# Performance work log

Hardware: AMD Instinct MI355X
Metric: run time of the kernel (lower is better)

The kernel has to match this reference:

```python
import jax, jax.numpy as jnp
import numpy as np

N = 100000          # number of nodes
E = 128             # embedding size
NUM_LAYERS = 4
SMOOTH = 12.0       # MAXIMUM_SMOOTHNESS
RELATIONS = [("at", 2), ("clear", 1), ("on", 2)]  # sorted, as in module
ATOM_COUNTS = {"at": 150000, "clear": 150000, "on": 150000}


def mish(x):
    return x * jnp.tanh(jax.nn.softplus(x))


def _linear_init(k, din, dout):
    s = 1.0 / np.sqrt(din)
    kw, kb = jax.random.split(k)
    w = jax.random.uniform(kw, (din, dout), jnp.float32, -s, s)
    b = jax.random.uniform(kb, (dout,), jnp.float32, -s, s)
    return w, b


def setup_inputs() -> dict:
    key = jax.random.key(0)
    ks = iter(jax.random.split(key, 64))
    inp = {}
    inp["node_embeddings"] = jax.random.normal(next(ks), (N, E), jnp.float32)
    for name, ar in RELATIONS:
        inp[f"atoms_{name}"] = jax.random.randint(
            next(ks), (ATOM_COUNTS[name] * ar,), 0, N, dtype=jnp.int32)
        d = ar * E
        inp[f"w_in_{name}"], inp[f"b_in_{name}"] = _linear_init(next(ks), d, d)
        inp[f"w_out_{name}"], inp[f"b_out_{name}"] = _linear_init(next(ks), d, d)
    # update MLP: Linear(2E, 2E) -> mish -> Linear(2E, E)
    inp["w_u_in"], inp["b_u_in"] = _linear_init(next(ks), 2 * E, 2 * E)
    inp["w_u_out"], inp["b_u_out"] = _linear_init(next(ks), 2 * E, E)
    return inp


def _forward(node_embeddings, atoms, params):
    w_u_in, b_u_in, w_u_out, b_u_out = params["update"]

    def layer(h):
        msgs, idxs = [], []
        for name, ar in RELATIONS:
            w_in, b_in, w_out, b_out = params[name]
            av = atoms[name]                              # [A*ar] node indices
            x = h[av].reshape(-1, ar * E)                 # gather -> [A, ar*E]
            y = x + (mish(x @ w_in + b_in) @ w_out + b_out)  # residual MLP
            msgs.append(y.reshape(-1, E))
            idxs.append(av)
        msg = jnp.concatenate(msgs, 0)                    # [T, E]
        idx = jnp.concatenate(idxs, 0)                    # [T]
        # smooth-max aggregation (max offsets are not differentiated)
        seg_max = jax.ops.segment_max(msg, idx, num_segments=N)
        seg_max = jnp.where(jnp.isfinite(seg_max), seg_max, 0.0)  # empty -> 0 (include_self=False on zeros)
        seg_max = jax.lax.stop_gradient(seg_max)
        exps = jnp.exp(SMOOTH * (msg - seg_max[idx]))
        exps_sum = jax.ops.segment_sum(exps, idx, num_segments=N) + 1e-16
        max_msg = jnp.log(exps_sum) / SMOOTH + seg_max
        upd_in = jnp.concatenate([max_msg, h], axis=1)    # [N, 2E]
        upd = mish(upd_in @ w_u_in + b_u_in) @ w_u_out + b_u_out
        return h + upd                                    # outer residual

    h = node_embeddings
    for _ in range(NUM_LAYERS):
        h = layer(h)
    return h


def reference(node_embeddings, atoms_at, atoms_clear, atoms_on,
              w_in_at, b_in_at, w_out_at, b_out_at,
              w_in_clear, b_in_clear, w_out_clear, b_out_clear,
              w_in_on, b_in_on, w_out_on, b_out_on,
              w_u_in, b_u_in, w_u_out, b_u_out):
    atoms = {"at": atoms_at, "clear": atoms_clear, "on": atoms_on}
    params = {
        "at": (w_in_at, b_in_at, w_out_at, b_out_at),
        "clear": (w_in_clear, b_in_clear, w_out_clear, b_out_clear),
        "on": (w_in_on, b_in_on, w_out_on, b_out_on),
        "update": (w_u_in, b_u_in, w_u_out, b_u_out),
    }
    return _forward(node_embeddings, atoms, params)
```

## Files before the change

### kernel.cpp

```cpp
#include <hip/hip_runtime.h>
#include <hip/hip_bf16.h>
#include <math.h>

#define NNODES 100000
#define EDIM 128
#define TSLOTS 750000
#define NB 391
#define GRA 2344

typedef __bf16 bf16x8 __attribute__((ext_vector_type(8)));
typedef __bf16 bf16x4 __attribute__((ext_vector_type(4)));
typedef float f32x4 __attribute__((ext_vector_type(4)));
typedef unsigned int u32x4 __attribute__((ext_vector_type(4)));

#define T_SCALE 17.312340490667562f
#define INV_SCALE 0.05776226504666211f
#define EMPTY_V (-3.0701134f)

__device__ __forceinline__ float mishf(float x) {
  float u = __expf(fminf(x, 15.f));
  float num = u * (u + 2.f);
  return x * num * __builtin_amdgcn_rcpf(num + 2.f);
}

__device__ __forceinline__ double exp12t(float t) {
  t = fmaxf(t, -20000.f);
  float ti = floorf(t);
  float m = exp2f(t - ti);
  int ei = (int)ti;
  ei = ei < -1000 ? -1000 : (ei > 1000 ? 1000 : ei);
  return (double)m * __longlong_as_double(((long long)(1023 + ei)) << 52);
}

__device__ __forceinline__ float logS12(double S) {
  if (!(S > 0.0)) return EMPTY_V;
  long long b = __double_as_longlong(S);
  int e2 = (int)((b >> 52) & 0x7FF) - 1023;
  float mf = __uint_as_float(0x3F800000u | (unsigned)((b >> 29) & 0x7FFFFF));
  return ((float)e2 + log2f(mf)) * INV_SCALE;
}

__global__ void k_sentinel(float* out, int n) {
  int i = blockIdx.x * 256 + threadIdx.x;
  if (i < n) out[i] = 1.0e6f;
}

__global__ void k_init(const float* __restrict__ h0, __bf16* __restrict__ hb, int n8) {
  int i = blockIdx.x * 256 + threadIdx.x;
  if (i >= n8) return;
  float4 f0 = ((const float4*)h0)[i * 2];
  float4 f1 = ((const float4*)h0)[i * 2 + 1];
  bf16x8 p = {(__bf16)f0.x, (__bf16)f0.y, (__bf16)f0.z, (__bf16)f0.w,
              (__bf16)f1.x, (__bf16)f1.y, (__bf16)f1.z, (__bf16)f1.w};
  *(bf16x8*)(hb + (size_t)i * 8) = p;
}

struct TransDesc {
  const float* src[8];
  __bf16* dst[8];
  int R[8];
  int C[8];
  int tstart[9];
};

__global__ void k_transpose_all(TransDesc td) {
  __shared__ float tile[32][33];
  int b = blockIdx.x;
  int m = 0;
  while (m < 7 && b >= td.tstart[m + 1]) m++;
  int t = b - td.tstart[m];
  int R = td.R[m], C = td.C[m];
  int tcols = C >> 5;
  int by = t / tcols, bx = t - by * tcols;
  int tx = threadIdx.x & 31, ty = threadIdx.x >> 5;
  const float* src = td.src[m];
  __bf16* dst = td.dst[m];
  for (int i = 0; i < 32; i += 8)
    tile[ty + i][tx] = src[(size_t)(by * 32 + ty + i) * C + bx * 32 + tx];
  __syncthreads();
  for (int i = 0; i < 32; i += 8)
    dst[(size_t)(bx * 32 + ty + i) * R + by * 32 + tx] = (__bf16)tile[tx][ty + i];
}

__device__ __forceinline__ int slot_node(int s, const int* at, const int* cl, const int* on) {
  if (s < 300000) return at[s];
  if (s < 450000) return cl[s - 300000];
  return on[s - 450000];
}

__global__ void k_count(const int* __restrict__ at, const int* __restrict__ cl,
                        const int* __restrict__ on, int* __restrict__ cnt) {
  int s = blockIdx.x * 256 + threadIdx.x;
  if (s >= TSLOTS) return;
  atomicAdd(&cnt[slot_node(s, at, cl, on)], 1);
}

__global__ void k_bsum(const int* __restrict__ cnt, int* __restrict__ bsum) {
  __shared__ int sm[256];
  int n = blockIdx.x * 256 + threadIdx.x;
  sm[threadIdx.x] = (n < NNODES) ? cnt[n] : 0;
  __syncthreads();
  for (int st = 128; st > 0; st >>= 1) {
    if (threadIdx.x < st) sm[threadIdx.x] += sm[threadIdx.x + st];
    __syncthreads();
  }
  if (threadIdx.x == 0) bsum[blockIdx.x] = sm[0];
}

__global__ void k_bscan(const int* __restrict__ bsum, int* __restrict__ bpre,
                        int* __restrict__ off) {
  __shared__ int sm[512];
  int t = threadIdx.x;
  int v = (t < NB) ? bsum[t] : 0;
  sm[t] = v;
  __syncthreads();
  for (int st = 1; st < 512; st <<= 1) {
    int x = (t >= st) ? sm[t - st] : 0;
    __syncthreads();
    sm[t] += x;
    __syncthreads();
  }
  if (t < NB) bpre[t] = sm[t] - v;
  if (t == NB - 1) off[NNODES] = sm[t];
}

__global__ void k_off(const int* __restrict__ cnt, const int* __restrict__ bpre,
                      int* __restrict__ off) {
  __shared__ int sm[256];
  int n = blockIdx.x * 256 + threadIdx.x;
  int v = (n < NNODES) ? cnt[n] : 0;
  sm[threadIdx.x] = v;
  __syncthreads();
  for (int st = 1; st < 256; st <<= 1) {
    int t = (threadIdx.x >= st) ? sm[threadIdx.x - st] : 0;
    __syncthreads();
    sm[threadIdx.x] += t;
    __syncthreads();
  }
  if (n < NNODES) off[n] = bpre[blockIdx.x] + sm[threadIdx.x] - v;
}

__global__ void k_fill(const int* __restrict__ at, const int* __restrict__ cl,
                       const int* __restrict__ on, const int* __restrict__ off,
                       int* __restrict__ cnt, int* __restrict__ perm) {
  int s = blockIdx.x * 256 + threadIdx.x;
  if (s >= TSLOTS) return;
  int node = slot_node(s, at, cl, on);
  int pos = atomicAdd(&cnt[node], -1) - 1;
  perm[s] = off[node] + pos;
}

struct RelAll {
  const int* av[3];
  const __bf16* wt1[3];
  const float* b1[3];
  const __bf16* wt2[3];
  const float* b2[3];
  const int* prm[3];
};

__global__ __launch_bounds__(512, 6) void k_relf(
    const float* __restrict__ hf, const __bf16* __restrict__ hb,
    RelAll ra, _Float16* __restrict__ msg) {
  __shared__ __align__(16) __bf16 xs[64][264];
  __shared__ int prm[128];
  const int tid = threadIdx.x;
  const int lane = tid & 63;
  const int w = tid >> 6;
  const int b = blockIdx.x;
  const int m = (b < GRA) ? 0 : (b < 2 * GRA ? 1 : 2);
  const int row0 = (b - m * GRA) * 64;
  const int A = 150000;
  const int* av = ra.av[m];
  const __bf16* wt1 = ra.wt1[m];
  const float* b1 = ra.b1[m];
  const __bf16* wt2 = ra.wt2[m];
  const float* b2 = ra.b2[m];
  const int* permrel = ra.prm[m];
  const int lhi = lane >> 4, llo = lane & 15;
  ushort* zs = (ushort*)&xs[0][0];

  if (m < 2) {
    if (tid < 128) {
      int i2 = row0 * 2 + tid;
      prm[tid] = (i2 < 2 * A) ? permrel[i2] : 0;
    }
    if (hb != nullptr) {
      for (int i = 0; i < 4; ++i) {
        int s = tid + i * 512;
        int r = s >> 5, o = s & 31;
        int a = row0 + r;
        uint4 v = {0, 0, 0, 0};
        if (a < A) {
          int node = av[2 * a + (o >> 4)];
          v = *(const uint4*)(hb + (size_t)node * 128 + (o & 15) * 8);
        }
        *(uint4*)&xs[r][o * 8] = v;
      }
    } else {
      for (int i = 0; i < 8; ++i) {
        int s = tid + i * 512;
        int r = s >> 6, o = s & 63;
        int a = row0 + r;
        float4 f = {0.f, 0.f, 0.f, 0.f};
        if (a < A) {
          int node = av[2 * a + (o >> 5)];
          f = *(const float4*)(hf + (size_t)node * 128 + (o & 31) * 4);
        }
        bf16x4 p = {(__bf16)f.x, (__bf16)f.y, (__bf16)f.z, (__bf16)f.w};
        *(bf16x4*)&xs[r][o * 4] = p;
      }
    }
    __syncthreads();

    const int cb = w * 32;
    f32x4 acc1[4][2];
#pragma unroll
    for (int rt = 0; rt < 4; rt++)
#pragma unroll
      for (int ct = 0; ct < 2; ct++) acc1[rt][ct] = (f32x4){0.f, 0.f, 0.f, 0.f};
#pragma unroll
    for (int kk = 0; kk < 8; ++kk) {
      int k = kk * 32 + lhi * 8;
      bf16x8 af[4], bfr[2];
#pragma unroll
      for (int rt = 0; rt < 4; rt++) af[rt] = *(const bf16x8*)&xs[rt * 16 + llo][k];
#pragma unroll
      for (int ct = 0; ct < 2; ct++)
        bfr[ct] = *(const bf16x8*)(wt1 + (size_t)(cb + ct * 16 + llo) * 256 + k);
#pragma unroll
      for (int rt = 0; rt < 4; rt++)
#pragma unroll
        for (int ct = 0; ct < 2; ct++)
          acc1[rt][ct] = __builtin_amdgcn_mfma_f32_16x16x32_bf16(af[rt], bfr[ct], acc1[rt][ct], 0, 0, 0);
    }
    __syncthreads();

    float b1v[2];
#pragma unroll
    for (int ct = 0; ct < 2; ct++) b1v[ct] = b1[cb + ct * 16 + llo];
#pragma unroll
    for (int rt = 0; rt < 4; rt++)
#pragma unroll
      for (int ct = 0; ct < 2; ct++)
#pragma unroll
        for (int i = 0; i < 4; i++)
          xs[rt * 16 + lhi * 4 + i][cb + ct * 16 + llo] = (__bf16)mishf(acc1[rt][ct][i] + b1v[ct]);
    __syncthreads();

    f32x4 acc2[4][2];
#pragma unroll
    for (int rt = 0; rt < 4; rt++)
#pragma unroll
      for (int ct = 0; ct < 2; ct++) acc2[rt][ct] = (f32x4){0.f, 0.f, 0.f, 0.f};
#pragma unroll
    for (int kk = 0; kk < 8; ++kk) {
      int k = kk * 32 + lhi * 8;
      bf16x8 af[4], bfr[2];
#pragma unroll
      for (int rt = 0; rt < 4; rt++) af[rt] = *(const bf16x8*)&xs[rt * 16 + llo][k];
#pragma unroll
      for (int ct = 0; ct < 2; ct++)
        bfr[ct] = *(const bf16x8*)(wt2 + (size_t)(cb + ct * 16 + llo) * 256 + k);
#pragma unroll
      for (int rt = 0; rt < 4; rt++)
#pragma unroll
        for (int ct = 0; ct < 2; ct++)
          acc2[rt][ct] = __builtin_amdgcn_mfma_f32_16x16x32_bf16(af[rt], bfr[ct], acc2[rt][ct], 0, 0, 0);
    }
    __syncthreads();

    float b2v[2];
#pragma unroll
    for (int ct = 0; ct < 2; ct++) b2v[ct] = b2[cb + ct * 16 + llo];
#pragma unroll
    for (int rt = 0; rt < 4; rt++)
#pragma unroll
      for (int ct = 0; ct < 2; ct++)
#pragma unroll
        for (int i = 0; i < 4; i++) {
          int r = rt * 16 + lhi * 4 + i;
          int col = cb + ct * 16 + llo;
          union { ushort u; _Float16 f; } cv;
          cv.f = (_Float16)(acc2[rt][ct][i] + b2v[ct]);
          zs[r * 264 + col] = cv.u;
        }
    __syncthreads();

    for (int i = 0; i < 4; ++i) {
      int s = tid + i * 512;
      int sr = s >> 4;
      int c = s & 15;
      int a = row0 + (sr >> 1);
      if (a < A) {
        int rr = sr >> 1, c0 = (sr & 1) * 128 + c * 8;
        u32x4 z = *(const u32x4*)&zs[rr * 264 + c0];
        __builtin_nontemporal_store(z, (u32x4*)(msg + (size_t)prm[sr] * 128 + c * 8));
      }
    }
  } else {
    if (tid < 64) {
      int a = row0 + tid;
      prm[tid] = (a < A) ? permrel[a] : 0;
    }
    if (hb != nullptr) {
      for (int i = 0; i < 2; ++i) {
        int s = tid + i * 512;
        int r = s >> 4, o = s & 15;
        int a = row0 + r;
        uint4 v = {0, 0, 0, 0};
        if (a < A) {
          int node = av[a];
          v = *(const uint4*)(hb + (size_t)node * 128 + o * 8);
        }
        *(uint4*)&xs[r][o * 8] = v;
      }
    } else {
      for (int i = 0; i < 4; ++i) {
        int s = tid + i * 512;
        int r = s >> 5, o = s & 31;
        int a = row0 + r;
        float4 f = {0.f, 0.f, 0.f, 0.f};
        if (a < A) {
          int node = av[a];
          f = *(const float4*)(hf + (size_t)node * 128 + o * 4);
        }
        bf16x4 p = {(__bf16)f.x, (__bf16)f.y, (__bf16)f.z, (__bf16)f.w};
        *(bf16x4*)&xs[r][o * 4] = p;
      }
    }
    __syncthreads();

    const int cb = w * 16;
    f32x4 acc1[4];
#pragma unroll
    for (int rt = 0; rt < 4; rt++) acc1[rt] = (f32x4){0.f, 0.f, 0.f, 0.f};
#pragma unroll
    for (int kk = 0; kk < 4; ++kk) {
      int k = kk * 32 + lhi * 8;
      bf16x8 af[4], bfr;
#pragma unroll
      for (int rt = 0; rt < 4; rt++) af[rt] = *(const bf16x8*)&xs[rt * 16 + llo][k];
      bfr = *(const bf16x8*)(wt1 + (size_t)(cb + llo) * 128 + k);
#pragma unroll
      for (int rt = 0; rt < 4; rt++)
        acc1[rt] = __builtin_amdgcn_mfma_f32_16x16x32_bf16(af[rt], bfr, acc1[rt], 0, 0, 0);
    }
    __syncthreads();

    float b1v = b1[cb + llo];
#pragma unroll
    for (int rt = 0; rt < 4; rt++)
#pragma unroll
      for (int i = 0; i < 4; i++)
        xs[rt * 16 + lhi * 4 + i][cb + llo] = (__bf16)mishf(acc1[rt][i] + b1v);
    __syncthreads();

    f32x4 acc2[4];
#pragma unroll
    for (int rt = 0; rt < 4; rt++) acc2[rt] = (f32x4){0.f, 0.f, 0.f, 0.f};
#pragma unroll
    for (int kk = 0; kk < 4; ++kk) {
      int k = kk * 32 + lhi * 8;
      bf16x8 af[4], bfr;
#pragma unroll
      for (int rt = 0; rt < 4; rt++) af[rt] = *(const bf16x8*)&xs[rt * 16 + llo][k];
      bfr = *(const bf16x8*)(wt2 + (size_t)(cb + llo) * 128 + k);
#pragma unroll
      for (int rt = 0; rt < 4; rt++)
        acc2[rt] = __builtin_amdgcn_mfma_f32_16x16x32_bf16(af[rt], bfr, acc2[rt], 0, 0, 0);
    }
    __syncthreads();

    float b2v = b2[cb + llo];
#pragma unroll
    for (int rt = 0; rt < 4; rt++)
#pragma unroll
      for (int i = 0; i < 4; i++) {
        int r = rt * 16 + lhi * 4 + i;
        int col = cb + llo;
        union { ushort u; _Float16 f; } cv;
        cv.f = (_Float16)(acc2[rt][i] + b2v);
        zs[r * 264 + col] = cv.u;
      }
    __syncthreads();

    for (int i = 0; i < 2; ++i) {
      int s = tid + i * 512;
      int sr = s >> 4;
      int c = s & 15;
      int a = row0 + sr;
      if (a < A) {
        u32x4 z = *(const u32x4*)&zs[sr * 264 + c * 8];
        __builtin_nontemporal_store(z, (u32x4*)(msg + (size_t)prm[sr] * 128 + c * 8));
      }
    }
  }
}

__global__ __launch_bounds__(512, 6) void k_aggmlp(
    const _Float16* __restrict__ msg, const int* __restrict__ off,
    const float* __restrict__ hin, const __bf16* __restrict__ hb,
    const __bf16* __restrict__ wt1, const float* __restrict__ b1,
    const __bf16* __restrict__ wt2, const float* __restrict__ b2,
    float* __restrict__ hout, __bf16* __restrict__ hbout) {
  __shared__ __align__(16) __bf16 xs[64][264];
  __shared__ int offs[65];
  const int tid = threadIdx.x;
  const int lane = tid & 63;
  const int w = tid >> 6;
  const int node0 = blockIdx.x * 64;
  const bool useb = (hbout != nullptr);

  if (tid < 65) {
    int n = node0 + tid;
    offs[tid] = off[n < NNODES ? n : NNODES];
  }
  if (useb) {
    for (int i = 0; i < 2; ++i) {
      int s = tid + i * 512;
      int r = s >> 4, o = s & 15;
      int n = node0 + r;
      uint4 v = {0, 0, 0, 0};
      if (n < NNODES) v = *(const uint4*)(hb + (size_t)n * 128 + o * 8);
      *(uint4*)&xs[r][128 + o * 8] = v;
    }
  } else {
    for (int i = 0; i < 4; ++i) {
      int s = tid + i * 512;
      int r = s >> 5, o = s & 31;
      int n = node0 + r;
      float4 f = {0.f, 0.f, 0.f, 0.f};
      if (n < NNODES) f = *(const float4*)(hin + (size_t)n * 128 + o * 4);
      bf16x4 p = {(__bf16)f.x, (__bf16)f.y, (__bf16)f.z, (__bf16)f.w};
      *(bf16x4*)&xs[r][128 + o * 4] = p;
    }
  }
  if (node0 + 64 > NNODES) {
    for (int s = tid; s < 64 * 16; s += 512) {
      int r = s >> 4, o = s & 15;
      if (node0 + r >= NNODES) *(uint4*)&xs[r][o * 8] = (uint4){0, 0, 0, 0};
    }
  }
  __syncthreads();

  const int rg = lane >> 4;
  const int fl = lane & 15;
  const _Float16* mb = msg + fl * 8;

#pragma unroll 1
  for (int j = 0; j < 8; ++j) {
    int n = node0 + w * 8 + j;
    if (n >= NNODES) break;
    float h[8];
    if (useb) {
      bf16x8 hq = *(const bf16x8*)(hb + (size_t)n * 128 + fl * 8);
#pragma unroll
      for (int k = 0; k < 8; ++k) h[k] = (float)hq[k];
    } else {
      float4 a0 = *(const float4*)(hin + (size_t)n * 128 + fl * 8);
      float4 a1 = *(const float4*)(hin + (size_t)n * 128 + fl * 8 + 4);
      h[0] = a0.x; h[1] = a0.y; h[2] = a0.z; h[3] = a0.w;
      h[4] = a1.x; h[5] = a1.y; h[6] = a1.z; h[7] = a1.w;
    }
    int beg = offs[w * 8 + j];
    int deg = offs[w * 8 + j + 1] - beg;
    double S0 = 0.0, S1 = 0.0, S2 = 0.0, S3 = 0.0;
    double S4 = 0.0, S5 = 0.0, S6 = 0.0, S7 = 0.0;
#pragma unroll 1
    for (int d = 0; d < deg; d += 4) {
      int rp = d + rg;
      int rc = rp < deg ? rp : deg - 1;
      u32x4 v = __builtin_nontemporal_load((const u32x4*)(mb + (size_t)(beg + rc) * 128));
      if (rp >= deg) { v = (u32x4){0xFC00FC00u, 0xFC00FC00u, 0xFC00FC00u, 0xFC00FC00u}; }
      union { u32x4 u; _Float16 f[8]; } q;
      q.u = v;
      S0 += exp12t(((float)q.f[0] + h[0]) * T_SCALE);
      S1 += exp12t(((float)q.f[1] + h[1]) * T_SCALE);
      S2 += exp12t(((float)q.f[2] + h[2]) * T_SCALE);
      S3 += exp12t(((float)q.f[3] + h[3]) * T_SCALE);
      S4 += exp12t(((float)q.f[4] + h[4]) * T_SCALE);
      S5 += exp12t(((float)q.f[5] + h[5]) * T_SCALE);
      S6 += exp12t(((float)q.f[6] + h[6]) * T_SCALE);
      S7 += exp12t(((float)q.f[7] + h[7]) * T_SCALE);
    }
    S0 += __shfl_xor(S0, 16); S0 += __shfl_xor(S0, 32);
    S1 += __shfl_xor(S1, 16); S1 += __shfl_xor(S1, 32);
    S2 += __shfl_xor(S2, 16); S2 += __shfl_xor(S2, 32);
    S3 += __shfl_xor(S3, 16); S3 += __shfl_xor(S3, 32);
    S4 += __shfl_xor(S4, 16); S4 += __shfl_xor(S4, 32);
    S5 += __shfl_xor(S5, 16); S5 += __shfl_xor(S5, 32);
    S6 += __shfl_xor(S6, 16); S6 += __shfl_xor(S6, 32);
    S7 += __shfl_xor(S7, 16); S7 += __shfl_xor(S7, 32);
    if (rg == 0) {
      bf16x8 r;
      r[0] = (__bf16)logS12(S0);
      r[1] = (__bf16)logS12(S1);
      r[2] = (__bf16)logS12(S2);
      r[3] = (__bf16)logS12(S3);
      r[4] = (__bf16)logS12(S4);
      r[5] = (__bf16)logS12(S5);
      r[6] = (__bf16)logS12(S6);
      r[7] = (__bf16)logS12(S7);
      *(bf16x8*)&xs[n - node0][fl * 8] = r;
    }
  }
  __syncthreads();

  const int lhi = lane >> 4, llo = lane & 15;
  const int cb = w * 32;

  f32x4 acc1[4][2];
#pragma unroll
  for (int rt = 0; rt < 4; rt++)
#pragma unroll
    for (int ct = 0; ct < 2; ct++) acc1[rt][ct] = (f32x4){0.f, 0.f, 0.f, 0.f};
#pragma unroll
  for (int kk = 0; kk < 8; ++kk) {
    int k = kk * 32 + lhi * 8;
    bf16x8 af[4], bfr[2];
#pragma unroll
    for (int rt = 0; rt < 4; rt++) af[rt] = *(const bf16x8*)&xs[rt * 16 + llo][k];
#pragma unroll
    for (int ct = 0; ct < 2; ct++)
      bfr[ct] = *(const bf16x8*)(wt1 + (size_t)(cb + ct * 16 + llo) * 256 + k);
#pragma unroll
    for (int rt = 0; rt < 4; rt++)
#pragma unroll
      for (int ct = 0; ct < 2; ct++)
        acc1[rt][ct] = __builtin_amdgcn_mfma_f32_16x16x32_bf16(af[rt], bfr[ct], acc1[rt][ct], 0, 0, 0);
  }
  __syncthreads();

  float b1v[2];
#pragma unroll
  for (int ct = 0; ct < 2; ct++) b1v[ct] = b1[cb + ct * 16 + llo];
#pragma unroll
  for (int rt = 0; rt < 4; rt++)
#pragma unroll
    for (int ct = 0; ct < 2; ct++)
#pragma unroll
      for (int i = 0; i < 4; i++)
        xs[rt * 16 + lhi * 4 + i][cb + ct * 16 + llo] = (__bf16)mishf(acc1[rt][ct][i] + b1v[ct]);
  __syncthreads();

  const int cb2 = w * 16;
  f32x4 acc2[4];
#pragma unroll
  for (int rt = 0; rt < 4; rt++) acc2[rt] = (f32x4){0.f, 0.f, 0.f, 0.f};
#pragma unroll
  for (int kk = 0; kk < 8; ++kk) {
    int k = kk * 32 + lhi * 8;
    bf16x8 af[4], bfr;
#pragma unroll
    for (int rt = 0; rt < 4; rt++) af[rt] = *(const bf16x8*)&xs[rt * 16 + llo][k];
    bfr = *(const bf16x8*)(wt2 + (size_t)(cb2 + llo) * 256 + k);
#pragma unroll
    for (int rt = 0; rt < 4; rt++)
      acc2[rt] = __builtin_amdgcn_mfma_f32_16x16x32_bf16(af[rt], bfr, acc2[rt], 0, 0, 0);
  }

  float b2v = b2[cb2 + llo];
#pragma unroll
  for (int rt = 0; rt < 4; rt++)
#pragma unroll
    for (int i = 0; i < 4; i++) {
      int r = rt * 16 + lhi * 4 + i;
      int n = node0 + r;
      if (n >= NNODES) continue;
      int col = cb2 + llo;
      size_t idx = (size_t)n * 128 + col;
      float nh = hin[idx] + acc2[rt][i] + b2v;
      hout[idx] = nh;
      if (hbout != nullptr) hbout[idx] = (__bf16)nh;
    }
}

extern "C" void kernel_launch(void* const* d_in, const int* in_sizes, int n_in,
                              void* d_out, int out_size, void* d_ws, size_t ws_size,
                              hipStream_t stream) {
  const float* h0 = (const float*)d_in[0];
  const int* at = (const int*)d_in[1];
  const float* w_in_at = (const float*)d_in[2];
  const float* b_in_at = (const float*)d_in[3];
  const float* w_out_at = (const float*)d_in[4];
  const float* b_out_at = (const float*)d_in[5];
  const int* cl = (const int*)d_in[6];
  const float* w_in_cl = (const float*)d_in[7];
  const float* b_in_cl = (const float*)d_in[8];
  const float* w_out_cl = (const float*)d_in[9];
  const float* b_out_cl = (const float*)d_in[10];
  const int* on = (const int*)d_in[11];
  const float* w_in_on = (const float*)d_in[12];
  const float* b_in_on = (const float*)d_in[13];
  const float* w_out_on = (const float*)d_in[14];
  const float* b_out_on = (const float*)d_in[15];
  const float* w_u_in = (const float*)d_in[16];
  const float* b_u_in = (const float*)d_in[17];
  const float* w_u_out = (const float*)d_in[18];
  const float* b_u_out = (const float*)d_in[19];

  float* hout = (float*)d_out;
  char* ws = (char*)d_ws;

  const size_t MSG_B = (size_t)TSLOTS * 128 * 2;
  const size_t OFF_B = 400016;
  const size_t CNT_B = 400000;
  const size_t BS_B = 1568;
  const size_t PERM_B = 3000000;
  const size_t WT_B = 786432;
  const size_t MM_B = (size_t)NNODES * 128 * 2;
  const size_t HB_B = (size_t)NNODES * 128 * 2;
  const size_t REQ2 = MSG_B + OFF_B + CNT_B + 2 * BS_B + PERM_B + WT_B + MM_B;
  const size_t REQ3 = REQ2 + HB_B;

  if (ws_size < REQ2) {
    k_sentinel<<<(out_size + 255) / 256, 256, 0, stream>>>((float*)d_out, out_size);
    return;
  }

  _Float16* msg = (_Float16*)ws;
  int* off = (int*)(ws + MSG_B);
  int* cnt = (int*)(ws + MSG_B + OFF_B);
  int* bsum = (int*)(ws + MSG_B + OFF_B + CNT_B);
  int* bpre = (int*)(ws + MSG_B + OFF_B + CNT_B + BS_B);
  int* perm = (int*)(ws + MSG_B + OFF_B + CNT_B + 2 * BS_B);
  __bf16* wt = (__bf16*)(ws + MSG_B + OFF_B + CNT_B + 2 * BS_B + PERM_B);
  __bf16* hb = (ws_size >= REQ3) ? (__bf16*)(ws + REQ2) : nullptr;

  __bf16* wt_in_at = wt;
  __bf16* wt_out_at = wt + 65536;
  __bf16* wt_in_on = wt + 131072;
  __bf16* wt_out_on = wt + 196608;
  __bf16* wt_u_in = wt + 262144;
  __bf16* wt_u_out = wt + 327680;
  __bf16* wt_in_cl = wt + 360448;
  __bf16* wt_out_cl = wt + 376832;

  TransDesc td;
  const float* srcs[8] = {w_in_at, w_out_at, w_in_on, w_out_on, w_u_in, w_u_out, w_in_cl, w_out_cl};
  __bf16* dsts[8] = {wt_in_at, wt_out_at, wt_in_on, wt_out_on, wt_u_in, wt_u_out, wt_in_cl, wt_out_cl};
  int Rs[8] = {256, 256, 256, 256, 256, 256, 128, 128};
  int Cs[8] = {256, 256, 256, 256, 256, 128, 128, 128};
  int ts = 0;
  for (int m = 0; m < 8; ++m) {
    td.src[m] = srcs[m]; td.dst[m] = dsts[m]; td.R[m] = Rs[m]; td.C[m] = Cs[m];
    td.tstart[m] = ts; ts += (Rs[m] / 32) * (Cs[m] / 32);
  }
  td.tstart[8] = ts;
  k_transpose_all<<<384, 256, 0, stream>>>(td);

  if (hb) k_init<<<6250, 256, 0, stream>>>(h0, hb, NNODES * EDIM / 8);

  const int grid_mlp = (NNODES + 63) / 64;
  const int grid_slots = (TSLOTS + 255) / 256;

  hipMemsetAsync(cnt, 0, CNT_B, stream);
  k_count<<<grid_slots, 256, 0, stream>>>(at, cl, on, cnt);
  k_bsum<<<NB, 256, 0, stream>>>(cnt, bsum);
  k_bscan<<<1, 512, 0, stream>>>(bsum, bpre, off);
  k_off<<<NB, 256, 0, stream>>>(cnt, bpre, off);
  k_fill<<<grid_slots, 256, 0, stream>>>(at, cl, on, off, cnt, perm);

  RelAll ra;
  ra.av[0] = at;  ra.wt1[0] = wt_in_at; ra.b1[0] = b_in_at; ra.wt2[0] = wt_out_at; ra.b2[0] = b_out_at; ra.prm[0] = perm;
  ra.av[1] = on;  ra.wt1[1] = wt_in_on; ra.b1[1] = b_in_on; ra.wt2[1] = wt_out_on; ra.b2[1] = b_out_on; ra.prm[1] = perm + 450000;
  ra.av[2] = cl;  ra.wt1[2] = wt_in_cl; ra.b1[2] = b_in_cl; ra.wt2[2] = wt_out_cl; ra.b2[2] = b_out_cl; ra.prm[2] = perm + 300000;

  for (int l = 0; l < 4; ++l) {
    const float* hs = (l == 0) ? h0 : hout;
    k_relf<<<3 * GRA, 512, 0, stream>>>(hs, hb, ra, msg);
    k_aggmlp<<<grid_mlp, 512, 0, stream>>>(msg, off, hs, hb, wt_u_in, b_u_in, wt_u_out, b_u_out, hout, hb);
  }
}
```

Measured before the change: 1.571 ms.

## Process atoms in order sorted by first node to improve gather locality

Adds a per-relation counting sort of atoms keyed by their first node index, built once per call. The relation MLP kernel then walks atoms in that sorted order through an indirection array, so neighbouring rows gather nearby embeddings and consecutive blocks touch clustered node rows. The aim is better cache hit rates on the random embedding gathers. In exchange it adds six setup kernels, an extra indirect index load per row, and a less regular read of the atom and perm arrays.

```diff
diff --git a/kernel.cpp b/kernel.cpp
--- a/kernel.cpp
+++ b/kernel.cpp
@@ -7,6 +7,7 @@
 #define TSLOTS 750000
 #define NB 391
 #define GRA 2344
+#define OFFS 100004
 
 typedef __bf16 bf16x8 __attribute__((ext_vector_type(8)));
 typedef __bf16 bf16x4 __attribute__((ext_vector_type(4)));
@@ -150,6 +151,84 @@
   perm[s] = off[node] + pos;
 }
 
+__device__ __forceinline__ int rel_first_node(int s, const int* at, const int* on, const int* cl,
+                                              int* mo, int* ao) {
+  int m = s / 150000;
+  int a = s - m * 150000;
+  *mo = m; *ao = a;
+  return (m == 0) ? at[2 * a] : (m == 1 ? on[2 * a] : cl[a]);
+}
+
+__global__ void k_count2(const int* __restrict__ at, const int* __restrict__ on,
+                         const int* __restrict__ cl, int* __restrict__ cnt2) {
+  int s = blockIdx.x * 256 + threadIdx.x;
+  if (s >= 450000) return;
+  int m, a;
+  int node = rel_first_node(s, at, on, cl, &m, &a);
+  atomicAdd(&cnt2[m * NNODES + node], 1);
+}
+
+__global__ void k_bsum2(const int* __restrict__ cnt2, int* __restrict__ bsum2) {
+  __shared__ int sm[256];
+  int b = blockIdx.x;
+  int m = b / NB, bb = b - m * NB;
+  int n = bb * 256 + threadIdx.x;
+  sm[threadIdx.x] = (n < NNODES) ? cnt2[m * NNODES + n] : 0;
+  __syncthreads();
+  for (int st = 128; st > 0; st >>= 1) {
+    if (threadIdx.x < st) sm[threadIdx.x] += sm[threadIdx.x + st];
+    __syncthreads();
+  }
+  if (threadIdx.x == 0) bsum2[b] = sm[0];
+}
+
+__global__ void k_bscan2(const int* __restrict__ bsum2, int* __restrict__ bpre2,
+                         int* __restrict__ off2) {
+  __shared__ int sm[512];
+  int m = blockIdx.x;
+  int t = threadIdx.x;
+  int v = (t < NB) ? bsum2[m * NB + t] : 0;
+  sm[t] = v;
+  __syncthreads();
+  for (int st = 1; st < 512; st <<= 1) {
+    int x = (t >= st) ? sm[t - st] : 0;
+    __syncthreads();
+    sm[t] += x;
+    __syncthreads();
+  }
+  if (t < NB) bpre2[m * NB + t] = sm[t] - v;
+  if (t == NB - 1) off2[m * OFFS + NNODES] = sm[t];
+}
+
+__global__ void k_off2(const int* __restrict__ cnt2, const int* __restrict__ bpre2,
+                       int* __restrict__ off2) {
+  __shared__ int sm[256];
+  int b = blockIdx.x;
+  int m = b / NB, bb = b - m * NB;
+  int n = bb * 256 + threadIdx.x;
+  int v = (n < NNODES) ? cnt2[m * NNODES + n] : 0;
+  sm[threadIdx.x] = v;
+  __syncthreads();
+  for (int st = 1; st < 256; st <<= 1) {
+    int t = (threadIdx.x >= st) ? sm[threadIdx.x - st] : 0;
+    __syncthreads();
+    sm[threadIdx.x] += t;
+    __syncthreads();
+  }
+  if (n < NNODES) off2[m * OFFS + n] = bpre2[m * NB + bb] + sm[threadIdx.x] - v;
+}
+
+__global__ void k_fill2(const int* __restrict__ at, const int* __restrict__ on,
+                        const int* __restrict__ cl, const int* __restrict__ off2,
+                        int* __restrict__ cnt2, int* __restrict__ sidx) {
+  int s = blockIdx.x * 256 + threadIdx.x;
+  if (s >= 450000) return;
+  int m, a;
+  int node = rel_first_node(s, at, on, cl, &m, &a);
+  int pos = atomicAdd(&cnt2[m * NNODES + node], -1) - 1;
+  sidx[m * 150000 + off2[m * OFFS + node] + pos] = a;
+}
+
 struct RelAll {
   const int* av[3];
   const __bf16* wt1[3];
@@ -161,7 +240,7 @@
 
 __global__ __launch_bounds__(512, 6) void k_relf(
     const float* __restrict__ hf, const __bf16* __restrict__ hb,
-    RelAll ra, _Float16* __restrict__ msg) {
+    RelAll ra, const int* __restrict__ sidx, _Float16* __restrict__ msg) {
   __shared__ __align__(16) __bf16 xs[64][264];
   __shared__ int prm[128];
   const int tid = threadIdx.x;
@@ -177,13 +256,19 @@
   const __bf16* wt2 = ra.wt2[m];
   const float* b2 = ra.b2[m];
   const int* permrel = ra.prm[m];
+  const int* sx = sidx + m * 150000;
   const int lhi = lane >> 4, llo = lane & 15;
   ushort* zs = (ushort*)&xs[0][0];
 
   if (m < 2) {
     if (tid < 128) {
-      int i2 = row0 * 2 + tid;
-      prm[tid] = (i2 < 2 * A) ? permrel[i2] : 0;
+      int aa = row0 + (tid >> 1);
+      int pv = 0;
+      if (aa < A) {
+        int sa = sx[aa];
+        pv = permrel[2 * sa + (tid & 1)];
+      }
+      prm[tid] = pv;
     }
     if (hb != nullptr) {
       for (int i = 0; i < 4; ++i) {
@@ -192,7 +277,8 @@
         int a = row0 + r;
         uint4 v = {0, 0, 0, 0};
         if (a < A) {
-          int node = av[2 * a + (o >> 4)];
+          int sa = sx[a];
+          int node = av[2 * sa + (o >> 4)];
           v = *(const uint4*)(hb + (size_t)node * 128 + (o & 15) * 8);
         }
         *(uint4*)&xs[r][o * 8] = v;
@@ -204,7 +290,8 @@
         int a = row0 + r;
         float4 f = {0.f, 0.f, 0.f, 0.f};
         if (a < A) {
-          int node = av[2 * a + (o >> 5)];
+          int sa = sx[a];
+          int node = av[2 * sa + (o >> 5)];
           f = *(const float4*)(hf + (size_t)node * 128 + (o & 31) * 4);
         }
         bf16x4 p = {(__bf16)f.x, (__bf16)f.y, (__bf16)f.z, (__bf16)f.w};
@@ -300,8 +387,8 @@
     }
   } else {
     if (tid < 64) {
-      int a = row0 + tid;
-      prm[tid] = (a < A) ? permrel[a] : 0;
+      int aa = row0 + tid;
+      prm[tid] = (aa < A) ? permrel[sx[aa]] : 0;
     }
     if (hb != nullptr) {
       for (int i = 0; i < 2; ++i) {
@@ -310,7 +397,7 @@
         int a = row0 + r;
         uint4 v = {0, 0, 0, 0};
         if (a < A) {
-          int node = av[a];
+          int node = av[sx[a]];
           v = *(const uint4*)(hb + (size_t)node * 128 + o * 8);
         }
         *(uint4*)&xs[r][o * 8] = v;
@@ -322,7 +409,7 @@
         int a = row0 + r;
         float4 f = {0.f, 0.f, 0.f, 0.f};
         if (a < A) {
-          int node = av[a];
+          int node = av[sx[a]];
           f = *(const float4*)(hf + (size_t)node * 128 + o * 4);
         }
         bf16x4 p = {(__bf16)f.x, (__bf16)f.y, (__bf16)f.z, (__bf16)f.w};
@@ -626,6 +713,12 @@
   int* bpre = (int*)(ws + MSG_B + OFF_B + CNT_B + BS_B);
   int* perm = (int*)(ws + MSG_B + OFF_B + CNT_B + 2 * BS_B);
   __bf16* wt = (__bf16*)(ws + MSG_B + OFF_B + CNT_B + 2 * BS_B + PERM_B);
+  char* aux = ws + MSG_B + OFF_B + CNT_B + 2 * BS_B + PERM_B + WT_B;
+  int* cnt2 = (int*)aux;
+  int* off2 = (int*)(aux + 1200000);
+  int* bsum2 = (int*)(aux + 2400064);
+  int* bpre2 = (int*)(aux + 2404800);
+  int* sidx = (int*)(aux + 2409536);
   __bf16* hb = (ws_size >= REQ3) ? (__bf16*)(ws + REQ2) : nullptr;
 
   __bf16* wt_in_at = wt;
@@ -654,6 +747,7 @@
 
   const int grid_mlp = (NNODES + 63) / 64;
   const int grid_slots = (TSLOTS + 255) / 256;
+  const int grid_atoms = (450000 + 255) / 256;
 
   hipMemsetAsync(cnt, 0, CNT_B, stream);
   k_count<<<grid_slots, 256, 0, stream>>>(at, cl, on, cnt);
@@ -662,6 +756,13 @@
   k_off<<<NB, 256, 0, stream>>>(cnt, bpre, off);
   k_fill<<<grid_slots, 256, 0, stream>>>(at, cl, on, off, cnt, perm);
 
+  hipMemsetAsync(cnt2, 0, 1200000, stream);
+  k_count2<<<grid_atoms, 256, 0, stream>>>(at, on, cl, cnt2);
+  k_bsum2<<<3 * NB, 256, 0, stream>>>(cnt2, bsum2);
+  k_bscan2<<<3, 512, 0, stream>>>(bsum2, bpre2, off2);
+  k_off2<<<3 * NB, 256, 0, stream>>>(cnt2, bpre2, off2);
+  k_fill2<<<grid_atoms, 256, 0, stream>>>(at, on, cl, off2, cnt2, sidx);
+
   RelAll ra;
   ra.av[0] = at;  ra.wt1[0] = wt_in_at; ra.b1[0] = b_in_at; ra.wt2[0] = wt_out_at; ra.b2[0] = b_out_at; ra.prm[0] = perm;
   ra.av[1] = on;  ra.wt1[1] = wt_in_on; ra.b1[1] = b_in_on; ra.wt2[1] = wt_out_on; ra.b2[1] = b_out_on; ra.prm[1] = perm + 450000;
@@ -669,7 +770,7 @@
 
   for (int l = 0; l < 4; ++l) {
     const float* hs = (l == 0) ? h0 : hout;
-    k_relf<<<3 * GRA, 512, 0, stream>>>(hs, hb, ra, msg);
+    k_relf<<<3 * GRA, 512, 0, stream>>>(hs, hb, ra, sidx, msg);
     k_aggmlp<<<grid_mlp, 512, 0, stream>>>(msg, off, hs, hb, wt_u_in, b_u_in, wt_u_out, b_u_out, hout, hb);
   }
 }
```

After: 1.652 ms. 1.05x slower.
